# Kernel tuning notes

Measured on AMD Instinct MI355X. Metric: run time of the kernel, lower is better.

## Reference

```python
import jax, jax.numpy as jnp
import numpy as np

jax.config.update("jax_enable_x64", True)

DIM0, DIM1 = 32, 32
D = DIM0 * DIM1
NUM_STATE = 2048
NUM_SQRTM = 6     # self._torch_logm = ('pade', 6, 8): 6 matrix square roots
PADE_ORDER = 8    # order-8 Gauss-Legendre Pade approximant of log


def _sphere(theta):
    # real (k, 2d) -> complex unit vectors (k, d) (Sphere 'quotient' map)
    d = theta.shape[-1] // 2
    z = theta[..., :d] + 1j * theta[..., d:]
    return z / jnp.linalg.norm(z, axis=-1, keepdims=True)


def _logm_psd_pade(A):
    # scaling: B = A^(1/2^s)  (principal root, == s repeated principal sqrtms)
    lam, V = jnp.linalg.eigh(A)
    lam = jnp.clip(lam, 1e-30, None)
    B = (V * (lam ** (1.0 / 2.0 ** NUM_SQRTM))) @ V.conj().T
    # Pade via Gauss-Legendre partial fractions: log(B) ~ sum_j w_j (I + x_j E)^{-1} E,  E = B - I
    t, w = np.polynomial.legendre.leggauss(PADE_ORDER)
    x = jnp.asarray((t + 1.0) / 2.0)
    w = jnp.asarray(w / 2.0)
    I = jnp.eye(A.shape[-1], dtype=A.dtype)
    E = B - I
    Ms = I[None, :, :] + x[:, None, None] * E[None, :, :]          # (P, d, d)
    sol = jnp.linalg.solve(Ms, jnp.broadcast_to(E, Ms.shape))      # (P, d, d)
    logB = jnp.sum(w[:, None, None] * sol, axis=0)
    return (2.0 ** NUM_SQRTM) * logB  # undo scaling


def _loss(theta_p, theta_psiA, theta_psiB, rho_target):
    p = jax.nn.softmax(theta_p.astype(jnp.float64))                # (k,)
    a = _sphere(theta_psiA.astype(jnp.float64))                    # (k, dim0) complex
    b = _sphere(theta_psiB.astype(jnp.float64))                    # (k, dim1) complex
    phi = jnp.einsum('ki,kj->kij', a, b).reshape(NUM_STATE, D)     # product states kron(a,b)
    rho = jnp.einsum('k,ki,kj->ij', p.astype(phi.dtype), phi, phi.conj())  # (D, D) PSD, tr=1
    log_rho = _logm_psd_pade(rho)
    # tr(rho_t log rho_t) (constant) - tr(rho_t log rho)
    lam_t = jnp.clip(jnp.linalg.eigvalsh(rho_target), 1e-18, None)
    tr_rho_log_rho = jnp.sum(lam_t * jnp.log(lam_t))
    return tr_rho_log_rho - jnp.trace(rho_target @ log_rho).real


def setup_inputs() -> dict:
    key = jax.random.key(0)
    k1, k2, k3, k4, k5 = jax.random.split(key, 5)
    theta_p = jax.random.normal(k1, (NUM_STATE,), dtype=jnp.float32)
    theta_psiA = jax.random.normal(k2, (NUM_STATE, 2 * DIM0), dtype=jnp.float32)
    theta_psiB = jax.random.normal(k3, (NUM_STATE, 2 * DIM1), dtype=jnp.float32)
    # random full-rank target density matrix (complex128 buffer, like set_dm_target)
    M = (jax.random.normal(k4, (D, D), dtype=jnp.float64)
         + 1j * jax.random.normal(k5, (D, D), dtype=jnp.float64))
    rho_t = M @ M.conj().T
    rho_t = rho_t / jnp.trace(rho_t).real
    return {"theta_p": theta_p, "theta_psiA": theta_psiA, "theta_psiB": theta_psiB,
            "rho_target": rho_t}


def reference(theta_p, theta_psiA, theta_psiB, rho_target):
    return _loss(theta_p, theta_psiA, theta_psiB, rho_target)
```

## Files before the change

kernel.cpp:

```cpp
#include <hip/hip_runtime.h>
#include <hip/hip_bf16.h>
#include <cmath>
#include <vector>


#define NM 1024
#define KST 2048
#define CHEB_R 13
#define CHEB_T 36
#define NS_STAGES 3
#define TAU_M 19
#define SLOTN (NM * NM)
#define SQ_BLOCKS 512

typedef double2 cplx;

#ifndef __has_builtin
#define __has_builtin(x) 0
#endif
#if __has_builtin(__builtin_amdgcn_mfma_f64_16x16x4f64)
#define HAVE_MFMA64 1
typedef double f64x4 __attribute__((ext_vector_type(4)));
#else
#define HAVE_MFMA64 0
#endif

__device__ double g_tr[160];
__device__ int    g_cfg[8];

static __device__ __forceinline__ cplx cmul(cplx a, cplx b) {
  return make_double2(a.x * b.x - a.y * b.y, a.x * b.y + a.y * b.x);
}
static __device__ __forceinline__ double ld_sc(const void* p, int w, long i) {
  if (w == 8) return ((const double*)p)[i];
  if (w == 4) return (double)((const float*)p)[i];
  return (double)__bfloat162float(((const __hip_bfloat16*)p)[i]);
}
static __device__ __forceinline__ unsigned int dual_word(float fv) {
  unsigned int F = __float_as_uint(fv);
  unsigned int b = ((F + 0x7FFFu + ((F >> 16) & 1u)) >> 16) & 0xFFFFu;
  return (b << 16) | b;
}
static __device__ __forceinline__ void atomAddD(double* p, double v) {
  __hip_atomic_fetch_add(p, v, __ATOMIC_RELAXED, __HIP_MEMORY_SCOPE_AGENT);
}

__global__ void mfma_probe_k() {
#if HAVE_MFMA64
  int l = threadIdx.x;
  double a = (double)((l & 15) + 17 * (l >> 4) + 1);
  double b = (double)(3 * (l >> 4) + 29 * (l & 15) + 2);
  f64x4 z = {0.0, 0.0, 0.0, 0.0};
  f64x4 d = __builtin_amdgcn_mfma_f64_16x16x4f64(a, b, z, 0, 0, 0);
  int ok[4] = {1, 1, 1, 1};
  #pragma unroll
  for (int g = 0; g < 4; ++g) {
    double v = d[g];
    int rr[4], cc[4];
    rr[0] = 4 * (l >> 4) + g;  cc[0] = l & 15;
    rr[1] = l & 15;            cc[1] = 4 * (l >> 4) + g;
    rr[2] = (l >> 4) + 4 * g;  cc[2] = l & 15;
    rr[3] = l & 15;            cc[3] = (l >> 4) + 4 * g;
    #pragma unroll
    for (int h = 0; h < 4; ++h) {
      double ref = 0.0;
      for (int k = 0; k < 4; ++k)
// ... 115 lines not shown
  if (threadIdx.x == 0) g_tr[slot] = red[0];
}

__global__ void softmax_sqrtp_k(const void* __restrict__ th, double* __restrict__ sqrtp) {
  __shared__ double red[256];
  int t = threadIdx.x, w = g_cfg[0];
  double mx = -1e300;
  for (int i = t; i < KST; i += 256) mx = fmax(mx, ld_sc(th, w, i));
  red[t] = mx; __syncthreads();
  for (int s = 128; s > 0; s >>= 1) { if (t < s) red[t] = fmax(red[t], red[t + s]); __syncthreads(); }
  double m = red[0]; __syncthreads();
  double sm = 0.0;
  for (int i = t; i < KST; i += 256) sm += exp(ld_sc(th, w, i) - m);
  red[t] = sm; __syncthreads();
  for (int s = 128; s > 0; s >>= 1) { if (t < s) red[t] += red[t + s]; __syncthreads(); }
  double Z = red[0];
  for (int i = t; i < KST; i += 256) sqrtp[i] = sqrt(exp(ld_sc(th, w, i) - m) / Z);
}

__global__ void normalize_rows_k(const void* __restrict__ thA, const void* __restrict__ thB,
                                 cplx* __restrict__ av, cplx* __restrict__ bv) {
  int rid = blockIdx.x * 8 + (threadIdx.x >> 5);
  int lane = threadIdx.x & 31;
  int which = rid >> 11, row = rid & 2047;
  const void* src = which ? thB : thA;
  int w = which ? g_cfg[2] : g_cfg[1];
  double re = ld_sc(src, w, (long)row * 64 + lane);
  double im = ld_sc(src, w, (long)row * 64 + lane + 32);
  double n2 = re * re + im * im;
  for (int off = 16; off > 0; off >>= 1) n2 += __shfl_down(n2, off, 32);
  n2 = __shfl(n2, 0, 32);
  double inv = (n2 > 0.0) ? 1.0 / sqrt(n2) : 0.0;
  (which ? bv : av)[(long)row * 32 + lane] = make_double2(re * inv, im * inv);
}

__global__ void build_C_k(const double* __restrict__ sqrtp, const cplx* __restrict__ av,
                          const cplx* __restrict__ bv, cplx* __restrict__ C) {
  __shared__ cplx as[32], bs[32];
  int k = blockIdx.x, t = threadIdx.x;
  if (t < 32) as[t] = av[k * 32 + t];
  else if (t < 64) bs[t - 32] = bv[k * 32 + (t - 32)];
  __syncthreads();
  double sp = sqrtp[k];
  for (int e = t; e < NM; e += 256) {
    cplx v = cmul(as[e >> 5], bs[e & 31]);
    C[(size_t)k * NM + e] = make_double2(sp * v.x, sp * v.y);
  }
}

__global__ __launch_bounds__(256) void gemm_rho_sq_k(const cplx* __restrict__ C,
                                                     cplx* __restrict__ D, double tauAdd) {
  __shared__ cplx LB[2][16][33];
  int bi = blockIdx.x >> 5, bj = blockIdx.x & 31;
  int r0 = bi * 64, c0 = bj * 32;
  int sel = g_cfg[6];
#if HAVE_MFMA64
  if (sel) {
    int lane = threadIdx.x & 63, w = threadIdx.x >> 6;
    int lr = lane & 15, lk = lane >> 4;
    int acol = r0 + 16 * w + lr;
    cplx ac[4], an[4], rbn[2];
    #pragma unroll
    for (int s = 0; s < 4; ++s) ac[s] = C[(size_t)(4 * s + lk) * NM + acol];
    #pragma unroll
    for (int q = 0; q < 2; ++q) {
      int e = threadIdx.x + q * 256;
      int kk = e >> 5, n = e & 31;
      LB[0][kk][n] = C[(size_t)kk * NM + c0 + n];
    }
    __syncthreads();
    f64x4 zz = {0.0, 0.0, 0.0, 0.0};
    f64x4 t1[2], t2[2], t3[2];
    #pragma unroll
    for (int j = 0; j < 2; ++j) { t1[j] = zz; t2[j] = zz; t3[j] = zz; }
    int cur = 0;
    for (int kt = 0; kt < KST; kt += 16) {
      bool more = kt + 16 < KST;
      if (more) {
        #pragma unroll
        for (int s = 0; s < 4; ++s)
          an[s] = C[(size_t)(kt + 16 + 4 * s + lk) * NM + acol];
        #pragma unroll
        for (int q = 0; q < 2; ++q) {
          int e = threadIdx.x + q * 256;
          int kk = e >> 5, n = e & 31;
          rbn[q] = C[(size_t)(kt + 16 + kk) * NM + c0 + n];
        }
      }
      #pragma unroll
      for (int s = 0; s < 4; ++s) {
        cplx a = ac[s];
        double ad = a.y - a.x;
        #pragma unroll
        for (int j = 0; j < 2; ++j) {
          cplx b = LB[cur][4 * s + lk][16 * j + lr];
          double bsm = b.x + b.y;
          t1[j] = __builtin_amdgcn_mfma_f64_16x16x4f64(a.x, b.x, t1[j], 0, 0, 0);
          t2[j] = __builtin_amdgcn_mfma_f64_16x16x4f64(a.y, b.y, t2[j], 0, 0, 0);
          t3[j] = __builtin_amdgcn_mfma_f64_16x16x4f64(ad, bsm, t3[j], 0, 0, 0);
        }
      }
      if (more) {
        #pragma unroll
        for (int q = 0; q < 2; ++q) {
          int e = threadIdx.x + q * 256;
          int kk = e >> 5, n = e & 31;
          LB[cur ^ 1][kk][n] = rbn[q];
        }
        #pragma unroll
        for (int s = 0; s < 4; ++s) ac[s] = an[s];
      }
      __syncthreads();
      cur ^= 1;
    }
    #pragma unroll
    for (int j = 0; j < 2; ++j)
      #pragma unroll
      for (int g = 0; g < 4; ++g) {
        int rr, cc; hyp_rc(sel, lk, lr, g, rr, cc);
        int r = r0 + 16 * w + rr, c = c0 + 16 * j + cc;
        double dx = t1[j][g] + t2[j][g];
        double dy = t3[j][g] + t1[j][g] - t2[j][g];
        if (r == c) { dx += tauAdd; dy = 0.0; }
        D[(size_t)r * NM + c] = make_double2(dx, dy);
      }
    return;
  }
#endif
  __shared__ cplx LA0[16][65];
  int tx = threadIdx.x & 15, ty = threadIdx.x >> 4;
  double ax[4][2] = {{0}}, ay[4][2] = {{0}};
  for (int kt = 0; kt < KST; kt += 16) {
    #pragma unroll
    for (int q = 0; q < 4; ++q) {
      int e = threadIdx.x + q * 256;
      int kk = e >> 6, m = e & 63;
      LA0[kk][m] = C[(size_t)(kt + kk) * NM + r0 + m];
    }
    #pragma unroll
    for (int q = 0; q < 2; ++q) {
      int e = threadIdx.x + q * 256;
      int kk = e >> 5, n = e & 31;
      LB[0][kk][n] = C[(size_t)(kt + kk) * NM + c0 + n];
    }
    __syncthreads();
    #pragma unroll
    for (int kk = 0; kk < 16; ++kk) {
      cplx af[4], bf[2];
      #pragma unroll
      for (int i = 0; i < 4; ++i) af[i] = LA0[kk][ty + 16 * i];
      #pragma unroll
      for (int j = 0; j < 2; ++j) bf[j] = LB[0][kk][tx + 16 * j];
      #pragma unroll
      for (int i = 0; i < 4; ++i)
        #pragma unroll
        for (int j = 0; j < 2; ++j) {
          ax[i][j] += af[i].x * bf[j].x + af[i].y * bf[j].y;
          ay[i][j] += af[i].y * bf[j].x - af[i].x * bf[j].y;
        }
    }
    __syncthreads();
  }
  #pragma unroll
  for (int i = 0; i < 4; ++i) {
    int r = r0 + ty + 16 * i;
    #pragma unroll
    for (int j = 0; j < 2; ++j) {
      int c = c0 + tx + 16 * j;
      double dx = ax[i][j], dy = ay[i][j];
      if (r == c) { dx += tauAdd; dy = 0.0; }
      D[(size_t)r * NM + c] = make_double2(dx, dy);
    }
  }
}

__global__ __launch_bounds__(256) void gemm_sq64c_k(const cplx* __restrict__ A,
                                                    const cplx* __restrict__ B,
                                                    cplx* __restrict__ D, double alpha,
                                                    double aS, double aD,
                                                    double bS, double bD,
                                                    const cplx* __restrict__ E,
                                                    double eBeta, int eMode,
                                                    const double* __restrict__ rt, int tidx) {
  __shared__ cplx LA[2][16][65];
  __shared__ cplx LB[2][16][33];
  __shared__ double red[256];
  int bi = blockIdx.x >> 5, bj = blockIdx.x & 31;
  int r0 = bi * 64, c0 = bj * 32;
  int sel = g_cfg[6];
  int tid = threadIdx.x;
  int amq = tid >> 4, akq = tid & 15;
  int bkq = tid >> 5, bnq = tid & 31;
#if HAVE_MFMA64
  if (sel) {
    int lane = tid & 63, w = tid >> 6;
    int lr = lane & 15, lk = lane >> 4;
    cplx raA[4], raB[2];
    #pragma unroll
    for (int q = 0; q < 4; ++q) {
      int m = amq + q * 16;
      cplx v = A[(size_t)(r0 + m) * NM + akq];
      int gr = r0 + m;
      LA[0][akq][m] = make_double2(aS * v.x + (gr == akq ? aD : 0.0), aS * v.y);
    }
    #pragma unroll
    for (int q = 0; q < 2; ++q) {
      int kk = bkq + q * 8;
      cplx v = B[(size_t)kk * NM + c0 + bnq];
      int gc = c0 + bnq;
      LB[0][kk][bnq] = make_double2(bS * v.x + (kk == gc ? bD : 0.0), bS * v.y);
    }
    __syncthreads();
    f64x4 zz = {0.0, 0.0, 0.0, 0.0};
    f64x4 t1[2], t2[2], t3[2];
    #pragma unroll
    for (int j = 0; j < 2; ++j) { t1[j] = zz; t2[j] = zz; t3[j] = zz; }
    int cur = 0;
    for (int kt = 0; kt < NM; kt += 16) {
      bool more = kt + 16 < NM;
      if (more) {
        #pragma unroll
        for (int q = 0; q < 4; ++q) {
          int m = amq + q * 16;
          raA[q] = A[(size_t)(r0 + m) * NM + kt + 16 + akq];
        }
        #pragma unroll
        for (int q = 0; q < 2; ++q) {
          int kk = bkq + q * 8;
          raB[q] = B[(size_t)(kt + 16 + kk) * NM + c0 + bnq];
        }
      }
      #pragma unroll
      for (int s = 0; s < 4; ++s) {
        cplx a = LA[cur][4 * s + lk][16 * w + lr];
        double as_ = a.x + a.y;
        #pragma unroll
        for (int j = 0; j < 2; ++j) {
          cplx b = LB[cur][4 * s + lk][16 * j + lr];
          double bs_ = b.x + b.y;
          t1[j] = __builtin_amdgcn_mfma_f64_16x16x4f64(a.x, b.x, t1[j], 0, 0, 0);
          t2[j] = __builtin_amdgcn_mfma_f64_16x16x4f64(a.y, b.y, t2[j], 0, 0, 0);
          t3[j] = __builtin_amdgcn_mfma_f64_16x16x4f64(as_, bs_, t3[j], 0, 0, 0);
        }
      }
      if (more) {
        #pragma unroll
        for (int q = 0; q < 4; ++q) {
          int m = amq + q * 16;
          int gr = r0 + m, gk = kt + 16 + akq;
          LA[cur ^ 1][akq][m] = make_double2(aS * raA[q].x + (gr == gk ? aD : 0.0),
                                             aS * raA[q].y);
        }
        #pragma unroll
        for (int q = 0; q < 2; ++q) {
          int kk = bkq + q * 8;
          int gk = kt + 16 + kk, gc = c0 + bnq;
          LB[cur ^ 1][kk][bnq] = make_double2(bS * raB[q].x + (gk == gc ? bD : 0.0),
                                              bS * raB[q].y);
        }
      }
      __syncthreads();
      cur ^= 1;
    }
    double tsum = 0.0;
    #pragma unroll
    for (int j = 0; j < 2; ++j)
      #pragma unroll
      for (int g = 0; g < 4; ++g) {
        int rr, cc; hyp_rc(sel, lk, lr, g, rr, cc);
        int r = r0 + 16 * w + rr, c = c0 + 16 * j + cc;
        double dx = alpha * (t1[j][g] - t2[j][g]);
        double dy = alpha * (t3[j][g] - t1[j][g] - t2[j][g]);
        if (tidx >= 0) tsum += rt[(size_t)r * NM + c] * dx;
        double ex = 0.0, ey = 0.0;
        if (eMode == 1) { cplx e = E[(size_t)r * NM + c]; ex = eBeta * e.x; ey = eBeta * e.y; }
        else if (eMode == 2 && r == c) ex = eBeta;
        D[(size_t)r * NM + c] = make_double2(dx + ex, dy + ey);
      }
    if (tidx >= 0) {
      red[tid] = tsum; __syncthreads();
      for (int st = 128; st > 0; st >>= 1) { if (tid < st) red[tid] += red[tid + st]; __syncthreads(); }
      if (tid == 0) atomAddD(&g_tr[tidx], red[0]);
    }
    return;
  }
#endif
  int tx = tid & 15, ty = tid >> 4;
  double ax[4][2] = {{0}}, ay[4][2] = {{0}};
  for (int kt = 0; kt < NM; kt += 16) {
    #pragma unroll
    for (int q = 0; q < 4; ++q) {
      int m = amq + q * 16;
      int gr = r0 + m, gk = kt + akq;
      cplx v = A[(size_t)(r0 + m) * NM + kt + akq];
      LA[0][akq][m] = make_double2(aS * v.x + (gr == gk ? aD : 0.0), aS * v.y);
    }
    #pragma unroll
    for (int q = 0; q < 2; ++q) {
      int kk = bkq + q * 8;
      int gk = kt + kk, gc = c0 + bnq;
      cplx v = B[(size_t)(kt + kk) * NM + c0 + bnq];
      LB[0][kk][bnq] = make_double2(bS * v.x + (gk == gc ? bD : 0.0), bS * v.y);
    }
    __syncthreads();
    #pragma unroll
    for (int kk = 0; kk < 16; ++kk) {
      cplx af[4], bf[2];
      #pragma unroll
      for (int i = 0; i < 4; ++i) af[i] = LA[0][kk][ty + 16 * i];
      #pragma unroll
      for (int j = 0; j < 2; ++j) bf[j] = LB[0][kk][tx + 16 * j];
      #pragma unroll
      for (int i = 0; i < 4; ++i)
        #pragma unroll
        for (int j = 0; j < 2; ++j) {
          ax[i][j] += af[i].x * bf[j].x - af[i].y * bf[j].y;
          ay[i][j] += af[i].x * bf[j].y + af[i].y * bf[j].x;
        }
    }
    __syncthreads();
  }
  double tsum = 0.0;
  #pragma unroll
  for (int i = 0; i < 4; ++i) {
    int r = r0 + ty + 16 * i;
    #pragma unroll
    for (int j = 0; j < 2; ++j) {
      int c = c0 + tx + 16 * j;
      double dx = alpha * ax[i][j], dy = alpha * ay[i][j];
      if (tidx >= 0) tsum += rt[(size_t)r * NM + c] * dx;
      double ex = 0.0, ey = 0.0;
      if (eMode == 1) { cplx e = E[(size_t)r * NM + c]; ex = eBeta * e.x; ey = eBeta * e.y; }
      else if (eMode == 2 && r == c) ex = eBeta;
      D[(size_t)r * NM + c] = make_double2(dx + ex, dy + ey);
    }
  }
  if (tidx >= 0) {
    red[tid] = tsum; __syncthreads();
    for (int st = 128; st > 0; st >>= 1) { if (tid < st) red[tid] += red[tid + st]; __syncthreads(); }
    if (tid == 0) atomAddD(&g_tr[tidx], red[0]);
  }
}

__global__ __launch_bounds__(256) void gemm_sq64r_k(const double* __restrict__ A,
                                                    const double* __restrict__ B,
                                                    double* __restrict__ D, double alpha,
                                                    const double* __restrict__ E,
                                                    double eBeta, int eMode) {
  __shared__ double LA[2][16][65];
  __shared__ double LB[2][16][33];
  int bi = blockIdx.x >> 5, bj = blockIdx.x & 31;
  int r0 = bi * 64, c0 = bj * 32;
  int sel = g_cfg[6];
  int tid = threadIdx.x;
  int amq = tid >> 4, akq = tid & 15;
  int bkq = tid >> 5, bnq = tid & 31;
#if HAVE_MFMA64
  if (sel) {
    int lane = tid & 63, w = tid >> 6;
    int lr = lane & 15, lk = lane >> 4;
    double raA[4], raB[2];
    #pragma unroll
    for (int q = 0; q < 4; ++q) {
      int m = amq + q * 16;
      LA[0][akq][m] = A[(size_t)(r0 + m) * NM + akq];
    }
    #pragma unroll
    for (int q = 0; q < 2; ++q) {
      int kk = bkq + q * 8;
      LB[0][kk][bnq] = B[(size_t)kk * NM + c0 + bnq];
    }
    __syncthreads();
    f64x4 zz = {0.0, 0.0, 0.0, 0.0};
    f64x4 acc[2];
    #pragma unroll
    for (int j = 0; j < 2; ++j) acc[j] = zz;
    int cur = 0;
    for (int kt = 0; kt < NM; kt += 16) {
      bool more = kt + 16 < NM;
      if (more) {
        #pragma unroll
        for (int q = 0; q < 4; ++q) {
          int m = amq + q * 16;
          raA[q] = A[(size_t)(r0 + m) * NM + kt + 16 + akq];
        }
        #pragma unroll
        for (int q = 0; q < 2; ++q) {
          int kk = bkq + q * 8;
          raB[q] = B[(size_t)(kt + 16 + kk) * NM + c0 + bnq];
        }
      }
      #pragma unroll
      for (int s = 0; s < 4; ++s) {
        double a = LA[cur][4 * s + lk][16 * w + lr];
        #pragma unroll
        for (int j = 0; j < 2; ++j) {
          double b = LB[cur][4 * s + lk][16 * j + lr];
          acc[j] = __builtin_amdgcn_mfma_f64_16x16x4f64(a, b, acc[j], 0, 0, 0);
        }
      }
      if (more) {
        #pragma unroll
        for (int q = 0; q < 4; ++q) {
          int m = amq + q * 16;
          LA[cur ^ 1][akq][m] = raA[q];
        }
        #pragma unroll
        for (int q = 0; q < 2; ++q) {
          int kk = bkq + q * 8;
          LB[cur ^ 1][kk][bnq] = raB[q];
        }
      }
      __syncthreads();
      cur ^= 1;
    }
    #pragma unroll
    for (int j = 0; j < 2; ++j)
      #pragma unroll
      for (int g = 0; g < 4; ++g) {
        int rr, cc; hyp_rc(sel, lk, lr, g, rr, cc);
        int r = r0 + 16 * w + rr, c = c0 + 16 * j + cc;
        double v = alpha * acc[j][g];
        if (eMode == 1) v += eBeta * E[(size_t)r * NM + c];
        else if (eMode == 2 && r == c) v += eBeta;
        D[(size_t)r * NM + c] = v;
      }
    return;
  }
#endif
  int tx = tid & 15, ty = tid >> 4;
  double acc[4][2] = {{0}};
  for (int kt = 0; kt < NM; kt += 16) {
    #pragma unroll
    for (int q = 0; q < 4; ++q) {
      int m = amq + q * 16;
      LA[0][akq][m] = A[(size_t)(r0 + m) * NM + kt + akq];
    }
    #pragma unroll
    for (int q = 0; q < 2; ++q) {
      int kk = bkq + q * 8;
      LB[0][kk][bnq] = B[(size_t)(kt + kk) * NM + c0 + bnq];
    }
    __syncthreads();
    #pragma unroll
    for (int kk = 0; kk < 16; ++kk) {
      double af[4], bf[2];
      #pragma unroll
      for (int i = 0; i < 4; ++i) af[i] = LA[0][kk][ty + 16 * i];
      #pragma unroll
      for (int j = 0; j < 2; ++j) bf[j] = LB[0][kk][tx + 16 * j];
      #pragma unroll
      for (int i = 0; i < 4; ++i)
        #pragma unroll
        for (int j = 0; j < 2; ++j) acc[i][j] += af[i] * bf[j];
    }
    __syncthreads();
  }
  #pragma unroll
  for (int i = 0; i < 4; ++i) {
    int r = r0 + ty + 16 * i;
    #pragma unroll
    for (int j = 0; j < 2; ++j) {
      int c = c0 + tx + 16 * j;
      double v = alpha * acc[i][j];
      if (eMode == 1) v += eBeta * E[(size_t)r * NM + c];
      else if (eMode == 2 && r == c) v += eBeta;
      D[(size_t)r * NM + c] = v;
    }
  }
}

__global__ void tau_dots_k(const double* __restrict__ T, const double* __restrict__ P, int i) {
  __shared__ double r1[256], r2[256], r3[256];
  double sTT = 0.0, sTP = 0.0, sDg = 0.0;
  #pragma unroll
  for (int q = 0; q < 8; ++q) {
    int e = blockIdx.x * 2048 + q * 256 + threadIdx.x;
    double v = T[e], w = P[e];
    sTT += v * v; sTP += v * w;
    if ((e >> 10) == (e & 1023)) sDg += v;
  }
  r1[threadIdx.x] = sTT; r2[threadIdx.x] = sTP; r3[threadIdx.x] = sDg;
  __syncthreads();
  for (int st = 128; st > 0; st >>= 1) {
    if (threadIdx.x < st) {
      r1[threadIdx.x] += r1[threadIdx.x + st];
      r2[threadIdx.x] += r2[threadIdx.x + st];
      r3[threadIdx.x] += r3[threadIdx.x + st];
    }
    __syncthreads();
  }
  if (threadIdx.x == 0) {
    atomAddD(&g_tr[90 + i], r1[0]);
    atomAddD(&g_tr[110 + i], r2[0]);
    atomAddD(&g_tr[64 + i], r3[0]);
  }
}

__global__ void ew_affine_k(cplx* X, double sc, double sh) {
  int idx = blockIdx.x * 256 + threadIdx.x;
  cplx v = X[idx];
  cplx o = make_double2(sc * v.x, sc * v.y);
  if ((idx >> 10) == (idx & 1023)) o.x += sh;
  X[idx] = o;
}

__global__ void ew_affine2_k(const cplx* __restrict__ S, cplx* __restrict__ D,
                             double sc, double sh) {
  int idx = blockIdx.x * 256 + threadIdx.x;
  cplx v = S[idx];
  cplx o = make_double2(sc * v.x, sc * v.y);
  if ((idx >> 10) == (idx & 1023)) o.x += sh;
  D[idx] = o;
}

__global__ void ew_affine_real_k(const double* __restrict__ rtr, double* __restrict__ X,
                                 double sc, double diagAdd) {
  int idx = blockIdx.x * 256 + threadIdx.x;
  double o = sc * rtr[idx];
  if ((idx >> 10) == (idx & 1023)) o += diagAdd;
// ... 270 lines not shown
```

Baseline: 11.82 ms.

## Shrink GEMM tiles to 32x32 and stream Hermitian A operand via registers

Changes the output tile of the rho-square and the square-matrix GEMMs from 64x32 to 32x32 and doubles the block count. Each wave now computes one 16x16 tile instead of two. The A operand is no longer staged in shared memory. It is read column-wise straight into registers, which relies on the matrices being Hermitian or symmetric (A[r][k] = conj(A[k][r])), and the conjugate and scaling are applied in registers. The aim is more parallelism across CUs and less LDS traffic, at the cost of less operand reuse per block and more global loads per flop, plus reliance on the symmetry assumption.

```diff
diff --git a/kernel.cpp b/kernel.cpp
--- a/kernel.cpp
+++ b/kernel.cpp
@@ -11,7 +11,7 @@
 #define NS_STAGES 3
 #define TAU_M 19
 #define SLOTN (NM * NM)
-#define SQ_BLOCKS 512
+#define SQ_BLOCKS 1024
 
 typedef double2 cplx;
 
@@ -233,27 +233,27 @@
                                                      cplx* __restrict__ D, double tauAdd) {
   __shared__ cplx LB[2][16][33];
   int bi = blockIdx.x >> 5, bj = blockIdx.x & 31;
-  int r0 = bi * 64, c0 = bj * 32;
+  int r0 = bi * 32, c0 = bj * 32;
   int sel = g_cfg[6];
+  int tid = threadIdx.x;
+  int bkq = tid >> 5, bnq = tid & 31;
 #if HAVE_MFMA64
   if (sel) {
-    int lane = threadIdx.x & 63, w = threadIdx.x >> 6;
+    int lane = tid & 63, w = tid >> 6;
+    int rq = w & 1, cq = w >> 1;
     int lr = lane & 15, lk = lane >> 4;
-    int acol = r0 + 16 * w + lr;
+    int acol = r0 + 16 * rq + lr;
     cplx ac[4], an[4], rbn[2];
     #pragma unroll
     for (int s = 0; s < 4; ++s) ac[s] = C[(size_t)(4 * s + lk) * NM + acol];
     #pragma unroll
     for (int q = 0; q < 2; ++q) {
-      int e = threadIdx.x + q * 256;
-      int kk = e >> 5, n = e & 31;
-      LB[0][kk][n] = C[(size_t)kk * NM + c0 + n];
+      int kk = bkq + q * 8;
+      LB[0][kk][bnq] = C[(size_t)kk * NM + c0 + bnq];
     }
     __syncthreads();
     f64x4 zz = {0.0, 0.0, 0.0, 0.0};
-    f64x4 t1[2], t2[2], t3[2];
-    #pragma unroll
-    for (int j = 0; j < 2; ++j) { t1[j] = zz; t2[j] = zz; t3[j] = zz; }
+    f64x4 t1 = zz, t2 = zz, t3 = zz;
     int cur = 0;
     for (int kt = 0; kt < KST; kt += 16) {
       bool more = kt + 16 < KST;
@@ -263,30 +263,25 @@
           an[s] = C[(size_t)(kt + 16 + 4 * s + lk) * NM + acol];
         #pragma unroll
         for (int q = 0; q < 2; ++q) {
-          int e = threadIdx.x + q * 256;
-          int kk = e >> 5, n = e & 31;
-          rbn[q] = C[(size_t)(kt + 16 + kk) * NM + c0 + n];
+          int kk = bkq + q * 8;
+          rbn[q] = C[(size_t)(kt + 16 + kk) * NM + c0 + bnq];
         }
       }
       #pragma unroll
       for (int s = 0; s < 4; ++s) {
         cplx a = ac[s];
         double ad = a.y - a.x;
-        #pragma unroll
-        for (int j = 0; j < 2; ++j) {
-          cplx b = LB[cur][4 * s + lk][16 * j + lr];
-          double bsm = b.x + b.y;
-          t1[j] = __builtin_amdgcn_mfma_f64_16x16x4f64(a.x, b.x, t1[j], 0, 0, 0);
-          t2[j] = __builtin_amdgcn_mfma_f64_16x16x4f64(a.y, b.y, t2[j], 0, 0, 0);
-          t3[j] = __builtin_amdgcn_mfma_f64_16x16x4f64(ad, bsm, t3[j], 0, 0, 0);
-        }
+        cplx b = LB[cur][4 * s + lk][16 * cq + lr];
+        double bsm = b.x + b.y;
+        t1 = __builtin_amdgcn_mfma_f64_16x16x4f64(a.x, b.x, t1, 0, 0, 0);
+        t2 = __builtin_amdgcn_mfma_f64_16x16x4f64(a.y, b.y, t2, 0, 0, 0);
+        t3 = __builtin_amdgcn_mfma_f64_16x16x4f64(ad, bsm, t3, 0, 0, 0);
       }
       if (more) {
         #pragma unroll
         for (int q = 0; q < 2; ++q) {
-          int e = threadIdx.x + q * 256;
-          int kk = e >> 5, n = e & 31;
-          LB[cur ^ 1][kk][n] = rbn[q];
+          int kk = bkq + q * 8;
+          LB[cur ^ 1][kk][bnq] = rbn[q];
         }
         #pragma unroll
         for (int s = 0; s < 4; ++s) ac[s] = an[s];
@@ -295,45 +290,36 @@
       cur ^= 1;
     }
     #pragma unroll
-    for (int j = 0; j < 2; ++j)
-      #pragma unroll
-      for (int g = 0; g < 4; ++g) {
-        int rr, cc; hyp_rc(sel, lk, lr, g, rr, cc);
-        int r = r0 + 16 * w + rr, c = c0 + 16 * j + cc;
-        double dx = t1[j][g] + t2[j][g];
-        double dy = t3[j][g] + t1[j][g] - t2[j][g];
-        if (r == c) { dx += tauAdd; dy = 0.0; }
-        D[(size_t)r * NM + c] = make_double2(dx, dy);
-      }
+    for (int g = 0; g < 4; ++g) {
+      int rr, cc; hyp_rc(sel, lk, lr, g, rr, cc);
+      int r = r0 + 16 * rq + rr, c = c0 + 16 * cq + cc;
+      double dx = t1[g] + t2[g];
+      double dy = t3[g] + t1[g] - t2[g];
+      if (r == c) { dx += tauAdd; dy = 0.0; }
+      D[(size_t)r * NM + c] = make_double2(dx, dy);
+    }
     return;
   }
 #endif
-  __shared__ cplx LA0[16][65];
-  int tx = threadIdx.x & 15, ty = threadIdx.x >> 4;
-  double ax[4][2] = {{0}}, ay[4][2] = {{0}};
+  int tx = tid & 15, ty = (tid >> 4) & 15;
+  double ax[2][2] = {{0}}, ay[2][2] = {{0}};
   for (int kt = 0; kt < KST; kt += 16) {
     #pragma unroll
-    for (int q = 0; q < 4; ++q) {
-      int e = threadIdx.x + q * 256;
-      int kk = e >> 6, m = e & 63;
-      LA0[kk][m] = C[(size_t)(kt + kk) * NM + r0 + m];
-    }
-    #pragma unroll
     for (int q = 0; q < 2; ++q) {
-      int e = threadIdx.x + q * 256;
-      int kk = e >> 5, n = e & 31;
-      LB[0][kk][n] = C[(size_t)(kt + kk) * NM + c0 + n];
+      int kk = bkq + q * 8;
+      LB[0][kk][bnq] = C[(size_t)(kt + kk) * NM + r0 + bnq];
+      LB[1][kk][bnq] = C[(size_t)(kt + kk) * NM + c0 + bnq];
     }
     __syncthreads();
     #pragma unroll
     for (int kk = 0; kk < 16; ++kk) {
-      cplx af[4], bf[2];
-      #pragma unroll
-      for (int i = 0; i < 4; ++i) af[i] = LA0[kk][ty + 16 * i];
-      #pragma unroll
-      for (int j = 0; j < 2; ++j) bf[j] = LB[0][kk][tx + 16 * j];
-      #pragma unroll
-      for (int i = 0; i < 4; ++i)
+      cplx af[2], bf[2];
+      #pragma unroll
+      for (int i = 0; i < 2; ++i) af[i] = LB[0][kk][ty + 16 * i];
+      #pragma unroll
+      for (int j = 0; j < 2; ++j) bf[j] = LB[1][kk][tx + 16 * j];
+      #pragma unroll
+      for (int i = 0; i < 2; ++i)
         #pragma unroll
         for (int j = 0; j < 2; ++j) {
           ax[i][j] += af[i].x * bf[j].x + af[i].y * bf[j].y;
@@ -343,7 +329,7 @@
     __syncthreads();
   }
   #pragma unroll
-  for (int i = 0; i < 4; ++i) {
+  for (int i = 0; i < 2; ++i) {
     int r = r0 + ty + 16 * i;
     #pragma unroll
     for (int j = 0; j < 2; ++j) {
@@ -363,27 +349,22 @@
                                                     const cplx* __restrict__ E,
                                                     double eBeta, int eMode,
                                                     const double* __restrict__ rt, int tidx) {
-  __shared__ cplx LA[2][16][65];
   __shared__ cplx LB[2][16][33];
   __shared__ double red[256];
   int bi = blockIdx.x >> 5, bj = blockIdx.x & 31;
-  int r0 = bi * 64, c0 = bj * 32;
+  int r0 = bi * 32, c0 = bj * 32;
   int sel = g_cfg[6];
   int tid = threadIdx.x;
-  int amq = tid >> 4, akq = tid & 15;
   int bkq = tid >> 5, bnq = tid & 31;
 #if HAVE_MFMA64
   if (sel) {
     int lane = tid & 63, w = tid >> 6;
+    int rq = w & 1, cq = w >> 1;
     int lr = lane & 15, lk = lane >> 4;
-    cplx raA[4], raB[2];
-    #pragma unroll
-    for (int q = 0; q < 4; ++q) {
-      int m = amq + q * 16;
-      cplx v = A[(size_t)(r0 + m) * NM + akq];
-      int gr = r0 + m;
-      LA[0][akq][m] = make_double2(aS * v.x + (gr == akq ? aD : 0.0), aS * v.y);
-    }
+    int rrow = r0 + 16 * rq + lr;
+    cplx ac[4], an[4], rbn[2];
+    #pragma unroll
+    for (int s = 0; s < 4; ++s) ac[s] = A[(size_t)(4 * s + lk) * NM + rrow];
     #pragma unroll
     for (int q = 0; q < 2; ++q) {
       int kk = bkq + q * 8;
@@ -393,71 +374,59 @@
     }
     __syncthreads();
     f64x4 zz = {0.0, 0.0, 0.0, 0.0};
-    f64x4 t1[2], t2[2], t3[2];
-    #pragma unroll
-    for (int j = 0; j < 2; ++j) { t1[j] = zz; t2[j] = zz; t3[j] = zz; }
+    f64x4 t1 = zz, t2 = zz, t3 = zz;
     int cur = 0;
     for (int kt = 0; kt < NM; kt += 16) {
       bool more = kt + 16 < NM;
       if (more) {
         #pragma unroll
-        for (int q = 0; q < 4; ++q) {
-          int m = amq + q * 16;
-          raA[q] = A[(size_t)(r0 + m) * NM + kt + 16 + akq];
-        }
+        for (int s = 0; s < 4; ++s)
+          an[s] = A[(size_t)(kt + 16 + 4 * s + lk) * NM + rrow];
         #pragma unroll
         for (int q = 0; q < 2; ++q) {
           int kk = bkq + q * 8;
-          raB[q] = B[(size_t)(kt + 16 + kk) * NM + c0 + bnq];
+          rbn[q] = B[(size_t)(kt + 16 + kk) * NM + c0 + bnq];
         }
       }
       #pragma unroll
       for (int s = 0; s < 4; ++s) {
-        cplx a = LA[cur][4 * s + lk][16 * w + lr];
-        double as_ = a.x + a.y;
-        #pragma unroll
-        for (int j = 0; j < 2; ++j) {
-          cplx b = LB[cur][4 * s + lk][16 * j + lr];
-          double bs_ = b.x + b.y;
-          t1[j] = __builtin_amdgcn_mfma_f64_16x16x4f64(a.x, b.x, t1[j], 0, 0, 0);
-          t2[j] = __builtin_amdgcn_mfma_f64_16x16x4f64(a.y, b.y, t2[j], 0, 0, 0);
-          t3[j] = __builtin_amdgcn_mfma_f64_16x16x4f64(as_, bs_, t3[j], 0, 0, 0);
-        }
+        int gk = kt + 4 * s + lk;
+        double axf = aS * ac[s].x + (rrow == gk ? aD : 0.0);
+        double ayf = -aS * ac[s].y;
+        double asm_ = axf + ayf;
+        cplx b = LB[cur][4 * s + lk][16 * cq + lr];
+        double bsm = b.x + b.y;
+        t1 = __builtin_amdgcn_mfma_f64_16x16x4f64(axf, b.x, t1, 0, 0, 0);
+        t2 = __builtin_amdgcn_mfma_f64_16x16x4f64(ayf, b.y, t2, 0, 0, 0);
+        t3 = __builtin_amdgcn_mfma_f64_16x16x4f64(asm_, bsm, t3, 0, 0, 0);
       }
       if (more) {
-        #pragma unroll
-        for (int q = 0; q < 4; ++q) {
-          int m = amq + q * 16;
-          int gr = r0 + m, gk = kt + 16 + akq;
-          LA[cur ^ 1][akq][m] = make_double2(aS * raA[q].x + (gr == gk ? aD : 0.0),
-                                             aS * raA[q].y);
-        }
         #pragma unroll
         for (int q = 0; q < 2; ++q) {
           int kk = bkq + q * 8;
           int gk = kt + 16 + kk, gc = c0 + bnq;
-          LB[cur ^ 1][kk][bnq] = make_double2(bS * raB[q].x + (gk == gc ? bD : 0.0),
-                                              bS * raB[q].y);
+          LB[cur ^ 1][kk][bnq] = make_double2(bS * rbn[q].x + (gk == gc ? bD : 0.0),
+                                              bS * rbn[q].y);
         }
+        #pragma unroll
+        for (int s = 0; s < 4; ++s) ac[s] = an[s];
       }
       __syncthreads();
       cur ^= 1;
     }
     double tsum = 0.0;
     #pragma unroll
-    for (int j = 0; j < 2; ++j)
-      #pragma unroll
-      for (int g = 0; g < 4; ++g) {
-        int rr, cc; hyp_rc(sel, lk, lr, g, rr, cc);
-        int r = r0 + 16 * w + rr, c = c0 + 16 * j + cc;
-        double dx = alpha * (t1[j][g] - t2[j][g]);
-        double dy = alpha * (t3[j][g] - t1[j][g] - t2[j][g]);
-        if (tidx >= 0) tsum += rt[(size_t)r * NM + c] * dx;
-        double ex = 0.0, ey = 0.0;
-        if (eMode == 1) { cplx e = E[(size_t)r * NM + c]; ex = eBeta * e.x; ey = eBeta * e.y; }
-        else if (eMode == 2 && r == c) ex = eBeta;
-        D[(size_t)r * NM + c] = make_double2(dx + ex, dy + ey);
-      }
+    for (int g = 0; g < 4; ++g) {
+      int rr, cc; hyp_rc(sel, lk, lr, g, rr, cc);
+      int r = r0 + 16 * rq + rr, c = c0 + 16 * cq + cc;
+      double dx = alpha * (t1[g] - t2[g]);
+      double dy = alpha * (t3[g] - t1[g] - t2[g]);
+      if (tidx >= 0) tsum += rt[(size_t)r * NM + c] * dx;
+      double ex = 0.0, ey = 0.0;
+      if (eMode == 1) { cplx e = E[(size_t)r * NM + c]; ex = eBeta * e.x; ey = eBeta * e.y; }
+      else if (eMode == 2 && r == c) ex = eBeta;
+      D[(size_t)r * NM + c] = make_double2(dx + ex, dy + ey);
+    }
     if (tidx >= 0) {
       red[tid] = tsum; __syncthreads();
       for (int st = 128; st > 0; st >>= 1) { if (tid < st) red[tid] += red[tid + st]; __syncthreads(); }
@@ -466,33 +435,32 @@
     return;
   }
 #endif
-  int tx = tid & 15, ty = tid >> 4;
-  double ax[4][2] = {{0}}, ay[4][2] = {{0}};
+  int tx = tid & 15, ty = (tid >> 4) & 15;
+  double ax[2][2] = {{0}}, ay[2][2] = {{0}};
   for (int kt = 0; kt < NM; kt += 16) {
-    #pragma unroll
-    for (int q = 0; q < 4; ++q) {
-      int m = amq + q * 16;
-      int gr = r0 + m, gk = kt + akq;
-      cplx v = A[(size_t)(r0 + m) * NM + kt + akq];
-      LA[0][akq][m] = make_double2(aS * v.x + (gr == gk ? aD : 0.0), aS * v.y);
-    }
     #pragma unroll
     for (int q = 0; q < 2; ++q) {
       int kk = bkq + q * 8;
-      int gk = kt + kk, gc = c0 + bnq;
-      cplx v = B[(size_t)(kt + kk) * NM + c0 + bnq];
-      LB[0][kk][bnq] = make_double2(bS * v.x + (gk == gc ? bD : 0.0), bS * v.y);
+      {
+        int gk = kt + kk, gr = r0 + bnq;
+        cplx v = A[(size_t)gk * NM + gr];
+        LB[0][kk][bnq] = make_double2(aS * v.x + (gr == gk ? aD : 0.0), -aS * v.y);
+      }
+      { int gk = kt + kk, gc = c0 + bnq;
+        cplx v = B[(size_t)gk * NM + gc];
+        LB[1][kk][bnq] = make_double2(bS * v.x + (gk == gc ? bD : 0.0), bS * v.y);
+      }
     }
     __syncthreads();
     #pragma unroll
     for (int kk = 0; kk < 16; ++kk) {
-      cplx af[4], bf[2];
-      #pragma unroll
-      for (int i = 0; i < 4; ++i) af[i] = LA[0][kk][ty + 16 * i];
-      #pragma unroll
-      for (int j = 0; j < 2; ++j) bf[j] = LB[0][kk][tx + 16 * j];
-      #pragma unroll
-      for (int i = 0; i < 4; ++i)
+      cplx af[2], bf[2];
+      #pragma unroll
+      for (int i = 0; i < 2; ++i) af[i] = LB[0][kk][ty + 16 * i];
+      #pragma unroll
+      for (int j = 0; j < 2; ++j) bf[j] = LB[1][kk][tx + 16 * j];
+      #pragma unroll
+      for (int i = 0; i < 2; ++i)
         #pragma unroll
         for (int j = 0; j < 2; ++j) {
           ax[i][j] += af[i].x * bf[j].x - af[i].y * bf[j].y;
@@ -503,7 +471,7 @@
   }
   double tsum = 0.0;
   #pragma unroll
-  for (int i = 0; i < 4; ++i) {
+  for (int i = 0; i < 2; ++i) {
     int r = r0 + ty + 16 * i;
     #pragma unroll
     for (int j = 0; j < 2; ++j) {
@@ -528,24 +496,21 @@
                                                     double* __restrict__ D, double alpha,
                                                     const double* __restrict__ E,
                                                     double eBeta, int eMode) {
-  __shared__ double LA[2][16][65];
   __shared__ double LB[2][16][33];
   int bi = blockIdx.x >> 5, bj = blockIdx.x & 31;
-  int r0 = bi * 64, c0 = bj * 32;
+  int r0 = bi * 32, c0 = bj * 32;
   int sel = g_cfg[6];
   int tid = threadIdx.x;
-  int amq = tid >> 4, akq = tid & 15;
   int bkq = tid >> 5, bnq = tid & 31;
 #if HAVE_MFMA64
   if (sel) {
     int lane = tid & 63, w = tid >> 6;
+    int rq = w & 1, cq = w >> 1;
     int lr = lane & 15, lk = lane >> 4;
-    double raA[4], raB[2];
-    #pragma unroll
-    for (int q = 0; q < 4; ++q) {
-      int m = amq + q * 16;
-      LA[0][akq][m] = A[(size_t)(r0 + m) * NM + akq];
-    }
+    int rrow = r0 + 16 * rq + lr;
+    double ac[4], an[4], rbn[2];
+    #pragma unroll
+    for (int s = 0; s < 4; ++s) ac[s] = A[(size_t)(4 * s + lk) * NM + rrow];
     #pragma unroll
     for (int q = 0; q < 2; ++q) {
       int kk = bkq + q * 8;
@@ -553,92 +518,76 @@
     }
     __syncthreads();
     f64x4 zz = {0.0, 0.0, 0.0, 0.0};
-    f64x4 acc[2];
-    #pragma unroll
-    for (int j = 0; j < 2; ++j) acc[j] = zz;
+    f64x4 acc = zz;
     int cur = 0;
     for (int kt = 0; kt < NM; kt += 16) {
       bool more = kt + 16 < NM;
       if (more) {
         #pragma unroll
-        for (int q = 0; q < 4; ++q) {
-          int m = amq + q * 16;
-          raA[q] = A[(size_t)(r0 + m) * NM + kt + 16 + akq];
-        }
+        for (int s = 0; s < 4; ++s)
+          an[s] = A[(size_t)(kt + 16 + 4 * s + lk) * NM + rrow];
         #pragma unroll
         for (int q = 0; q < 2; ++q) {
           int kk = bkq + q * 8;
-          raB[q] = B[(size_t)(kt + 16 + kk) * NM + c0 + bnq];
+          rbn[q] = B[(size_t)(kt + 16 + kk) * NM + c0 + bnq];
         }
       }
       #pragma unroll
       for (int s = 0; s < 4; ++s) {
-        double a = LA[cur][4 * s + lk][16 * w + lr];
-        #pragma unroll
-        for (int j = 0; j < 2; ++j) {
-          double b = LB[cur][4 * s + lk][16 * j + lr];
-          acc[j] = __builtin_amdgcn_mfma_f64_16x16x4f64(a, b, acc[j], 0, 0, 0);
-        }
+        double a = ac[s];
+        double b = LB[cur][4 * s + lk][16 * cq + lr];
+        acc = __builtin_amdgcn_mfma_f64_16x16x4f64(a, b, acc, 0, 0, 0);
       }
       if (more) {
-        #pragma unroll
-        for (int q = 0; q < 4; ++q) {
-          int m = amq + q * 16;
-          LA[cur ^ 1][akq][m] = raA[q];
-        }
         #pragma unroll
         for (int q = 0; q < 2; ++q) {
           int kk = bkq + q * 8;
-          LB[cur ^ 1][kk][bnq] = raB[q];
+          LB[cur ^ 1][kk][bnq] = rbn[q];
         }
+        #pragma unroll
+        for (int s = 0; s < 4; ++s) ac[s] = an[s];
       }
       __syncthreads();
       cur ^= 1;
     }
     #pragma unroll
-    for (int j = 0; j < 2; ++j)
-      #pragma unroll
-      for (int g = 0; g < 4; ++g) {
-        int rr, cc; hyp_rc(sel, lk, lr, g, rr, cc);
-        int r = r0 + 16 * w + rr, c = c0 + 16 * j + cc;
-        double v = alpha * acc[j][g];
-        if (eMode == 1) v += eBeta * E[(size_t)r * NM + c];
-        else if (eMode == 2 && r == c) v += eBeta;
-        D[(size_t)r * NM + c] = v;
-      }
+    for (int g = 0; g < 4; ++g) {
+      int rr, cc; hyp_rc(sel, lk, lr, g, rr, cc);
+      int r = r0 + 16 * rq + rr, c = c0 + 16 * cq + cc;
+      double v = alpha * acc[g];
+      if (eMode == 1) v += eBeta * E[(size_t)r * NM + c];
+      else if (eMode == 2 && r == c) v += eBeta;
+      D[(size_t)r * NM + c] = v;
+    }
     return;
   }
 #endif
-  int tx = tid & 15, ty = tid >> 4;
-  double acc[4][2] = {{0}};
+  int tx = tid & 15, ty = (tid >> 4) & 15;
+  double acc[2][2] = {{0}};
   for (int kt = 0; kt < NM; kt += 16) {
-    #pragma unroll
-    for (int q = 0; q < 4; ++q) {
-      int m = amq + q * 16;
-      LA[0][akq][m] = A[(size_t)(r0 + m) * NM + kt + akq];
-    }
     #pragma unroll
     for (int q = 0; q < 2; ++q) {
       int kk = bkq + q * 8;
-      LB[0][kk][bnq] = B[(size_t)(kt + kk) * NM + c0 + bnq];
+      LB[0][kk][bnq] = A[(size_t)(kt + kk) * NM + r0 + bnq];
+      LB[1][kk][bnq] = B[(size_t)(kt + kk) * NM + c0 + bnq];
     }
     __syncthreads();
     #pragma unroll
     for (int kk = 0; kk < 16; ++kk) {
-      double af[4], bf[2];
-      #pragma unroll
-      for (int i = 0; i < 4; ++i) af[i] = LA[0][kk][ty + 16 * i];
-      #pragma unroll
-      for (int j = 0; j < 2; ++j) bf[j] = LB[0][kk][tx + 16 * j];
-      #pragma unroll
-      for (int i = 0; i < 4; ++i)
+      double af[2], bf[2];
+      #pragma unroll
+      for (int i = 0; i < 2; ++i) af[i] = LB[0][kk][ty + 16 * i];
+      #pragma unroll
+      for (int j = 0; j < 2; ++j) bf[j] = LB[1][kk][tx + 16 * j];
+      #pragma unroll
+      for (int i = 0; i < 2; ++i)
         #pragma unroll
         for (int j = 0; j < 2; ++j) acc[i][j] += af[i] * bf[j];
     }
     __syncthreads();
   }
   #pragma unroll
-  for (int i = 0; i < 4; ++i) {
+  for (int i = 0; i < 2; ++i) {
     int r = r0 + ty + 16 * i;
     #pragma unroll
     for (int j = 0; j < 2; ++j) {
```

Measured after the change: 12.64 ms. 1.07x slower.

## Load A operand directly to registers using Hermitian symmetry, deepen K tile

Applied to the files above, without the earlier changes.

The complex and real square GEMM kernels now read A column-wise as its conjugate transpose. This relies on A being Hermitian (or symmetric in the real case), so the coalesced loads can feed MFMA operands straight from registers and the A tile no longer goes through shared memory. The K step is doubled to 32, which halves the number of barriers, and the B tile grows to match. The aim is to cut LDS traffic and synchronisation per flop. It costs more registers for the A prefetch, and results are wrong for any caller whose A is not Hermitian.

```diff
diff --git a/kernel.cpp b/kernel.cpp
--- a/kernel.cpp
+++ b/kernel.cpp
@@ -363,29 +363,23 @@
                                                     const cplx* __restrict__ E,
                                                     double eBeta, int eMode,
                                                     const double* __restrict__ rt, int tidx) {
-  __shared__ cplx LA[2][16][65];
-  __shared__ cplx LB[2][16][33];
+  __shared__ cplx LB[2][32][33];
   __shared__ double red[256];
   int bi = blockIdx.x >> 5, bj = blockIdx.x & 31;
   int r0 = bi * 64, c0 = bj * 32;
   int sel = g_cfg[6];
   int tid = threadIdx.x;
-  int amq = tid >> 4, akq = tid & 15;
   int bkq = tid >> 5, bnq = tid & 31;
 #if HAVE_MFMA64
   if (sel) {
     int lane = tid & 63, w = tid >> 6;
     int lr = lane & 15, lk = lane >> 4;
-    cplx raA[4], raB[2];
+    int rrow = r0 + 16 * w + lr;
+    cplx ac[8], an[8], rbn[4];
+    #pragma unroll
+    for (int s = 0; s < 8; ++s) ac[s] = A[(size_t)(4 * s + lk) * NM + rrow];
     #pragma unroll
     for (int q = 0; q < 4; ++q) {
-      int m = amq + q * 16;
-      cplx v = A[(size_t)(r0 + m) * NM + akq];
-      int gr = r0 + m;
-      LA[0][akq][m] = make_double2(aS * v.x + (gr == akq ? aD : 0.0), aS * v.y);
-    }
-    #pragma unroll
-    for (int q = 0; q < 2; ++q) {
       int kk = bkq + q * 8;
       cplx v = B[(size_t)kk * NM + c0 + bnq];
       int gc = c0 + bnq;
@@ -397,48 +391,43 @@
     #pragma unroll
     for (int j = 0; j < 2; ++j) { t1[j] = zz; t2[j] = zz; t3[j] = zz; }
     int cur = 0;
-    for (int kt = 0; kt < NM; kt += 16) {
-      bool more = kt + 16 < NM;
+    for (int kt = 0; kt < NM; kt += 32) {
+      bool more = kt + 32 < NM;
       if (more) {
         #pragma unroll
+        for (int s = 0; s < 8; ++s)
+          an[s] = A[(size_t)(kt + 32 + 4 * s + lk) * NM + rrow];
+        #pragma unroll
         for (int q = 0; q < 4; ++q) {
-          int m = amq + q * 16;
-          raA[q] = A[(size_t)(r0 + m) * NM + kt + 16 + akq];
-        }
-        #pragma unroll
-        for (int q = 0; q < 2; ++q) {
           int kk = bkq + q * 8;
-          raB[q] = B[(size_t)(kt + 16 + kk) * NM + c0 + bnq];
-        }
-      }
-      #pragma unroll
-      for (int s = 0; s < 4; ++s) {
-        cplx a = LA[cur][4 * s + lk][16 * w + lr];
-        double as_ = a.x + a.y;
+          rbn[q] = B[(size_t)(kt + 32 + kk) * NM + c0 + bnq];
+        }
+      }
+      #pragma unroll
+      for (int s = 0; s < 8; ++s) {
+        int gk = kt + 4 * s + lk;
+        double axf = aS * ac[s].x + (rrow == gk ? aD : 0.0);
+        double ayf = -aS * ac[s].y;
+        double asm_ = axf + ayf;
         #pragma unroll
         for (int j = 0; j < 2; ++j) {
           cplx b = LB[cur][4 * s + lk][16 * j + lr];
-          double bs_ = b.x + b.y;
-          t1[j] = __builtin_amdgcn_mfma_f64_16x16x4f64(a.x, b.x, t1[j], 0, 0, 0);
-          t2[j] = __builtin_amdgcn_mfma_f64_16x16x4f64(a.y, b.y, t2[j], 0, 0, 0);
-          t3[j] = __builtin_amdgcn_mfma_f64_16x16x4f64(as_, bs_, t3[j], 0, 0, 0);
+          double bsm = b.x + b.y;
+          t1[j] = __builtin_amdgcn_mfma_f64_16x16x4f64(axf, b.x, t1[j], 0, 0, 0);
+          t2[j] = __builtin_amdgcn_mfma_f64_16x16x4f64(ayf, b.y, t2[j], 0, 0, 0);
+          t3[j] = __builtin_amdgcn_mfma_f64_16x16x4f64(asm_, bsm, t3[j], 0, 0, 0);
         }
       }
       if (more) {
         #pragma unroll
         for (int q = 0; q < 4; ++q) {
-          int m = amq + q * 16;
-          int gr = r0 + m, gk = kt + 16 + akq;
-          LA[cur ^ 1][akq][m] = make_double2(aS * raA[q].x + (gr == gk ? aD : 0.0),
-                                             aS * raA[q].y);
-        }
-        #pragma unroll
-        for (int q = 0; q < 2; ++q) {
           int kk = bkq + q * 8;
-          int gk = kt + 16 + kk, gc = c0 + bnq;
-          LB[cur ^ 1][kk][bnq] = make_double2(bS * raB[q].x + (gk == gc ? bD : 0.0),
-                                              bS * raB[q].y);
-        }
+          int gk = kt + 32 + kk, gc = c0 + bnq;
+          LB[cur ^ 1][kk][bnq] = make_double2(bS * rbn[q].x + (gk == gc ? bD : 0.0),
+                                              bS * rbn[q].y);
+        }
+        #pragma unroll
+        for (int s = 0; s < 8; ++s) ac[s] = an[s];
       }
       __syncthreads();
       cur ^= 1;
@@ -466,60 +455,67 @@
     return;
   }
 #endif
-  int tx = tid & 15, ty = tid >> 4;
-  double ax[4][2] = {{0}}, ay[4][2] = {{0}};
-  for (int kt = 0; kt < NM; kt += 16) {
-    #pragma unroll
-    for (int q = 0; q < 4; ++q) {
-      int m = amq + q * 16;
-      int gr = r0 + m, gk = kt + akq;
-      cplx v = A[(size_t)(r0 + m) * NM + kt + akq];
-      LA[0][akq][m] = make_double2(aS * v.x + (gr == gk ? aD : 0.0), aS * v.y);
-    }
-    #pragma unroll
-    for (int q = 0; q < 2; ++q) {
-      int kk = bkq + q * 8;
-      int gk = kt + kk, gc = c0 + bnq;
-      cplx v = B[(size_t)(kt + kk) * NM + c0 + bnq];
-      LB[0][kk][bnq] = make_double2(bS * v.x + (gk == gc ? bD : 0.0), bS * v.y);
-    }
-    __syncthreads();
-    #pragma unroll
-    for (int kk = 0; kk < 16; ++kk) {
-      cplx af[4], bf[2];
-      #pragma unroll
-      for (int i = 0; i < 4; ++i) af[i] = LA[0][kk][ty + 16 * i];
-      #pragma unroll
-      for (int j = 0; j < 2; ++j) bf[j] = LB[0][kk][tx + 16 * j];
-      #pragma unroll
-      for (int i = 0; i < 4; ++i)
-        #pragma unroll
-        for (int j = 0; j < 2; ++j) {
-          ax[i][j] += af[i].x * bf[j].x - af[i].y * bf[j].y;
-          ay[i][j] += af[i].x * bf[j].y + af[i].y * bf[j].x;
-        }
-    }
-    __syncthreads();
-  }
-  double tsum = 0.0;
-  #pragma unroll
-  for (int i = 0; i < 4; ++i) {
-    int r = r0 + ty + 16 * i;
-    #pragma unroll
-    for (int j = 0; j < 2; ++j) {
-      int c = c0 + tx + 16 * j;
-      double dx = alpha * ax[i][j], dy = alpha * ay[i][j];
-      if (tidx >= 0) tsum += rt[(size_t)r * NM + c] * dx;
-      double ex = 0.0, ey = 0.0;
-      if (eMode == 1) { cplx e = E[(size_t)r * NM + c]; ex = eBeta * e.x; ey = eBeta * e.y; }
-      else if (eMode == 2 && r == c) ex = eBeta;
-      D[(size_t)r * NM + c] = make_double2(dx + ex, dy + ey);
-    }
-  }
-  if (tidx >= 0) {
-    red[tid] = tsum; __syncthreads();
-    for (int st = 128; st > 0; st >>= 1) { if (tid < st) red[tid] += red[tid + st]; __syncthreads(); }
-    if (tid == 0) atomAddD(&g_tr[tidx], red[0]);
+  {
+    cplx* As = &LB[0][0][0];
+    cplx* Bs = &LB[1][0][0];
+    int tx = tid & 15, ty = tid >> 4;
+    double ax[4][2] = {{0}}, ay[4][2] = {{0}};
+    for (int kt = 0; kt < NM; kt += 16) {
+      #pragma unroll
+      for (int q = 0; q < 2; ++q) {
+        int kk = (tid >> 5) + q * 8;
+        {
+          int gk = kt + kk;
+          #pragma unroll
+          for (int h = 0; h < 2; ++h) {
+            int m = bnq + 32 * h, gr = r0 + m;
+            cplx v = A[(size_t)gk * NM + gr];
+            As[kk * 65 + m] = make_double2(aS * v.x + (gr == gk ? aD : 0.0), -aS * v.y);
+          }
+        }
+        { int gk = kt + kk, gc = c0 + bnq;
+          cplx v = B[(size_t)gk * NM + gc];
+          Bs[kk * 33 + bnq] = make_double2(bS * v.x + (gk == gc ? bD : 0.0), bS * v.y);
+        }
+      }
+      __syncthreads();
+      #pragma unroll
+      for (int kk = 0; kk < 16; ++kk) {
+        cplx af[4], bf[2];
+        #pragma unroll
+        for (int i = 0; i < 4; ++i) af[i] = As[kk * 65 + ty + 16 * i];
+        #pragma unroll
+        for (int j = 0; j < 2; ++j) bf[j] = Bs[kk * 33 + tx + 16 * j];
+        #pragma unroll
+        for (int i = 0; i < 4; ++i)
+          #pragma unroll
+          for (int j = 0; j < 2; ++j) {
+            ax[i][j] += af[i].x * bf[j].x - af[i].y * bf[j].y;
+            ay[i][j] += af[i].x * bf[j].y + af[i].y * bf[j].x;
+          }
+      }
+      __syncthreads();
+    }
+    double tsum = 0.0;
+    #pragma unroll
+    for (int i = 0; i < 4; ++i) {
+      int r = r0 + ty + 16 * i;
+      #pragma unroll
+      for (int j = 0; j < 2; ++j) {
+        int c = c0 + tx + 16 * j;
+        double dx = alpha * ax[i][j], dy = alpha * ay[i][j];
+        if (tidx >= 0) tsum += rt[(size_t)r * NM + c] * dx;
+        double ex = 0.0, ey = 0.0;
+        if (eMode == 1) { cplx e = E[(size_t)r * NM + c]; ex = eBeta * e.x; ey = eBeta * e.y; }
+        else if (eMode == 2 && r == c) ex = eBeta;
+        D[(size_t)r * NM + c] = make_double2(dx + ex, dy + ey);
+      }
+    }
+    if (tidx >= 0) {
+      red[tid] = tsum; __syncthreads();
+      for (int st = 128; st > 0; st >>= 1) { if (tid < st) red[tid] += red[tid + st]; __syncthreads(); }
+      if (tid == 0) atomAddD(&g_tr[tidx], red[0]);
+    }
   }
 }
 
@@ -528,26 +524,22 @@
                                                     double* __restrict__ D, double alpha,
                                                     const double* __restrict__ E,
                                                     double eBeta, int eMode) {
-  __shared__ double LA[2][16][65];
-  __shared__ double LB[2][16][33];
+  __shared__ double LB[2][32][33];
   int bi = blockIdx.x >> 5, bj = blockIdx.x & 31;
   int r0 = bi * 64, c0 = bj * 32;
   int sel = g_cfg[6];
   int tid = threadIdx.x;
-  int amq = tid >> 4, akq = tid & 15;
   int bkq = tid >> 5, bnq = tid & 31;
 #if HAVE_MFMA64
   if (sel) {
     int lane = tid & 63, w = tid >> 6;
     int lr = lane & 15, lk = lane >> 4;
-    double raA[4], raB[2];
+    int rrow = r0 + 16 * w + lr;
+    double ac[8], an[8], rbn[4];
+    #pragma unroll
+    for (int s = 0; s < 8; ++s) ac[s] = A[(size_t)(4 * s + lk) * NM + rrow];
     #pragma unroll
     for (int q = 0; q < 4; ++q) {
-      int m = amq + q * 16;
-      LA[0][akq][m] = A[(size_t)(r0 + m) * NM + akq];
-    }
-    #pragma unroll
-    for (int q = 0; q < 2; ++q) {
       int kk = bkq + q * 8;
       LB[0][kk][bnq] = B[(size_t)kk * NM + c0 + bnq];
     }
@@ -557,23 +549,21 @@
     #pragma unroll
     for (int j = 0; j < 2; ++j) acc[j] = zz;
     int cur = 0;
-    for (int kt = 0; kt < NM; kt += 16) {
-      bool more = kt + 16 < NM;
+    for (int kt = 0; kt < NM; kt += 32) {
+      bool more = kt + 32 < NM;
       if (more) {
         #pragma unroll
+        for (int s = 0; s < 8; ++s)
+          an[s] = A[(size_t)(kt + 32 + 4 * s + lk) * NM + rrow];
+        #pragma unroll
         for (int q = 0; q < 4; ++q) {
-          int m = amq + q * 16;
-          raA[q] = A[(size_t)(r0 + m) * NM + kt + 16 + akq];
-        }
-        #pragma unroll
-        for (int q = 0; q < 2; ++q) {
           int kk = bkq + q * 8;
-          raB[q] = B[(size_t)(kt + 16 + kk) * NM + c0 + bnq];
-        }
-      }
-      #pragma unroll
-      for (int s = 0; s < 4; ++s) {
-        double a = LA[cur][4 * s + lk][16 * w + lr];
+          rbn[q] = B[(size_t)(kt + 32 + kk) * NM + c0 + bnq];
+        }
+      }
+      #pragma unroll
+      for (int s = 0; s < 8; ++s) {
+        double a = ac[s];
         #pragma unroll
         for (int j = 0; j < 2; ++j) {
           double b = LB[cur][4 * s + lk][16 * j + lr];
@@ -583,14 +573,11 @@
       if (more) {
         #pragma unroll
         for (int q = 0; q < 4; ++q) {
-          int m = amq + q * 16;
-          LA[cur ^ 1][akq][m] = raA[q];
-        }
-        #pragma unroll
-        for (int q = 0; q < 2; ++q) {
           int kk = bkq + q * 8;
-          LB[cur ^ 1][kk][bnq] = raB[q];
-        }
+          LB[cur ^ 1][kk][bnq] = rbn[q];
+        }
+        #pragma unroll
+        for (int s = 0; s < 8; ++s) ac[s] = an[s];
       }
       __syncthreads();
       cur ^= 1;
@@ -609,44 +596,49 @@
     return;
   }
 #endif
-  int tx = tid & 15, ty = tid >> 4;
-  double acc[4][2] = {{0}};
-  for (int kt = 0; kt < NM; kt += 16) {
-    #pragma unroll
-    for (int q = 0; q < 4; ++q) {
-      int m = amq + q * 16;
-      LA[0][akq][m] = A[(size_t)(r0 + m) * NM + kt + akq];
-    }
-    #pragma unroll
-    for (int q = 0; q < 2; ++q) {
-      int kk = bkq + q * 8;
-      LB[0][kk][bnq] = B[(size_t)(kt + kk) * NM + c0 + bnq];
-    }
-    __syncthreads();
-    #pragma unroll
-    for (int kk = 0; kk < 16; ++kk) {
-      double af[4], bf[2];
-      #pragma unroll
-      for (int i = 0; i < 4; ++i) af[i] = LA[0][kk][ty + 16 * i];
-      #pragma unroll
-      for (int j = 0; j < 2; ++j) bf[j] = LB[0][kk][tx + 16 * j];
-      #pragma unroll
-      for (int i = 0; i < 4; ++i)
-        #pragma unroll
-        for (int j = 0; j < 2; ++j) acc[i][j] += af[i] * bf[j];
-    }
-    __syncthreads();
-  }
-  #pragma unroll
-  for (int i = 0; i < 4; ++i) {
-    int r = r0 + ty + 16 * i;
-    #pragma unroll
-    for (int j = 0; j < 2; ++j) {
-      int c = c0 + tx + 16 * j;
-      double v = alpha * acc[i][j];
-      if (eMode == 1) v += eBeta * E[(size_t)r * NM + c];
-      else if (eMode == 2 && r == c) v += eBeta;
-      D[(size_t)r * NM + c] = v;
+  {
+    double* As = &LB[0][0][0];
+    double* Bs = &LB[1][0][0];
+    int tx = tid & 15, ty = tid >> 4;
+    double acc[4][2] = {{0}};
+    for (int kt = 0; kt < NM; kt += 16) {
+      #pragma unroll
+      for (int q = 0; q < 2; ++q) {
+        int kk = (tid >> 5) + q * 8;
+        int gk = kt + kk;
+        #pragma unroll
+        for (int h = 0; h < 2; ++h) {
+          int m = bnq + 32 * h;
+          As[kk * 65 + m] = A[(size_t)gk * NM + r0 + m];
+        }
+        Bs[kk * 33 + bnq] = B[(size_t)gk * NM + c0 + bnq];
+      }
+      __syncthreads();
+      #pragma unroll
+      for (int kk = 0; kk < 16; ++kk) {
+        double af[4], bf[2];
+        #pragma unroll
+        for (int i = 0; i < 4; ++i) af[i] = As[kk * 65 + ty + 16 * i];
+        #pragma unroll
+        for (int j = 0; j < 2; ++j) bf[j] = Bs[kk * 33 + tx + 16 * j];
+        #pragma unroll
+        for (int i = 0; i < 4; ++i)
+          #pragma unroll
+          for (int j = 0; j < 2; ++j) acc[i][j] += af[i] * bf[j];
+      }
+      __syncthreads();
+    }
+    #pragma unroll
+    for (int i = 0; i < 4; ++i) {
+      int r = r0 + ty + 16 * i;
+      #pragma unroll
+      for (int j = 0; j < 2; ++j) {
+        int c = c0 + tx + 16 * j;
+        double v = alpha * acc[i][j];
+        if (eMode == 1) v += eBeta * E[(size_t)r * NM + c];
+        else if (eMode == 2 && r == c) v += eBeta;
+        D[(size_t)r * NM + c] = v;
+      }
     }
   }
 }
```

Measured after the change: 11.13 ms. -5.9%, faster.
